# Performance work log

Measured on AMD Instinct MI355X. Metric: run time of the kernel, lower is better.

## Reference

```python
import jax, jax.numpy as jnp
import numpy as np

B, N, F = 4, 100000, 64   # batch, points per cloud, feature dim
S, K = 256, 8             # render size, points per pixel
RADIUS = 1.0
R = 2.0 * RADIUS / float(S)  # self.r in the torch module


def setup_inputs() -> dict:
    key = jax.random.key(0)
    k1, k2, k3, k4 = jax.random.split(key, 4)
    features = jax.random.normal(k1, (B, N, F), dtype=jnp.float32)
    # packed point indices (rasterizer output); all valid here
    idx = jax.random.randint(k2, (B, S, S, K), 0, B * N, dtype=jnp.int64)
    zbuf = jax.random.uniform(k3, (B, S, S, K), dtype=jnp.float32)
    # squared xy distances, scaled into [0, r^2) so exp weights are non-trivial
    dist_xy = jax.random.uniform(k4, (B, S, S, K), dtype=jnp.float32) * (R * R)
    return {"features": features, "idx": idx, "zbuf": zbuf, "dist_xy": dist_xy}


def reference(features, idx, zbuf, dist_xy):
    r = R
    # exponential_alpha: permute to (B, K, S, S), normalize by r^2, exp
    d = jnp.transpose(dist_xy, (0, 3, 1, 2))                 # B,K,S,S
    alpha = jnp.exp(-jnp.maximum(d / (r * r), 0.0))
    weights = jnp.clip(alpha, 0.0, 0.99)

    idx_p = jnp.transpose(idx, (0, 3, 1, 2))                 # B,K,S,S (long)
    valid = (idx_p >= 0).astype(features.dtype)

    feats_packed = features.reshape(B * N, F)                # packed features

    # alpha_composite: front-to-back over K with transmittance
    w_eff = weights * valid                                  # B,K,S,S
    trans = jnp.cumprod(1.0 - w_eff, axis=1)
    trans = jnp.concatenate([jnp.ones_like(trans[:, :1]), trans[:, :-1]], axis=1)
    contrib = w_eff * trans                                  # B,K,S,S

    safe_idx = jnp.clip(idx_p, 0, B * N - 1)
    out = jnp.zeros((B, F, S, S), dtype=features.dtype)
    for k in range(K):  # K is a small fixed constant (8)
        g = feats_packed[safe_idx[:, k]]                     # B,S,S,F gather
        out = out + jnp.transpose(g, (0, 3, 1, 2)) * contrib[:, k][:, None]

    # normalized depth: w_normed = (weights*valid) / sum_k, z_weighted
    w_sum = jnp.maximum(jnp.sum(w_eff, axis=1, keepdims=True), 1e-9)
    w_normed = w_eff / w_sum
    z = jnp.transpose(zbuf, (0, 3, 1, 2))                    # B,K,S,S
    depth = jnp.sum(z * w_normed, axis=1, keepdims=True)     # B,1,S,S

    # concat composited feats (B,F,S,S) with depth (B,1,S,S)
    return jnp.concatenate([out, depth], axis=1)
```

## Files before the change

kernel.cpp:

```cpp
#include <hip/hip_runtime.h>


#define BB 4
#define NN 100000
#define FF 64
#define SS 256
#define KK 8
#define BN (BB * NN)
#define RR_INV 16384.0f

__global__ __launch_bounds__(256)
void points_render_kernel(const float* __restrict__ features,
                          const int*   __restrict__ idx,
                          const float* __restrict__ zbuf,
                          const float* __restrict__ dist,
                          float* __restrict__ out)
{
    __shared__ float tile[64][FF + 1];
    __shared__ float s_contrib[64][KK];
    __shared__ int   s_off[64][KK];

    const int tid  = threadIdx.x;
    const int wave = tid >> 6;
    const int lane = tid & 63;

    const int blk = blockIdx.x;
    const int xb  = blk & 3;
    const int y   = (blk >> 2) & (SS - 1);
    const int b   = blk >> 10;
    const int x0  = xb * 64;

    const long long pixbase = (((long long)b * SS + y) * SS + x0);

    if (tid < 64) {
        const long long p = pixbase + tid;
        const float4* d4 = (const float4*)(dist + p * KK);
        const float4* z4 = (const float4*)(zbuf + p * KK);
        const int4*   i4 = (const int4*)(idx  + p * KK);
        float4 da = d4[0], db = d4[1];
        float4 za = z4[0], zb = z4[1];
        int4   ia = i4[0], ib = i4[1];

        float dd[KK] = {da.x, da.y, da.z, da.w, db.x, db.y, db.z, db.w};
        float zz[KK] = {za.x, za.y, za.z, za.w, zb.x, zb.y, zb.z, zb.w};
        int   ii[KK] = {ia.x, ia.y, ia.z, ia.w, ib.x, ib.y, ib.z, ib.w};

        float trans = 1.0f, wsum = 0.0f, depth = 0.0f;
        #pragma unroll
        for (int k = 0; k < KK; ++k) {
            float a  = __expf(-fmaxf(dd[k] * RR_INV, 0.0f));
            float we = fminf(a, 0.99f);
            if (ii[k] < 0) we = 0.0f;
            s_contrib[tid][k] = we * trans;
            trans *= (1.0f - we);
            wsum  += we;
            depth += zz[k] * we;

            int si = ii[k];
            si = si < 0 ? 0 : (si > BN - 1 ? BN - 1 : si);
            s_off[tid][k] = si * FF;
        }
        tile[tid][FF] = depth / fmaxf(wsum, 1e-9f);
    }
    __syncthreads();

    const float* fl = features + lane;

    #pragma unroll 4
    for (int i = 0; i < 16; ++i) {
        const int xl = wave * 16 + i;
        const float4 c0 = *(const float4*)&s_contrib[xl][0];
        const float4 c1 = *(const float4*)&s_contrib[xl][4];
        const int4   o0 = *(const int4*)&s_off[xl][0];
        const int4   o1 = *(const int4*)&s_off[xl][4];

        const float g0 = fl[o0.x], g1 = fl[o0.y], g2 = fl[o0.z], g3 = fl[o0.w];
        const float g4 = fl[o1.x], g5 = fl[o1.y], g6 = fl[o1.z], g7 = fl[o1.w];

        tile[xl][lane] = g0*c0.x + g1*c0.y + g2*c0.z + g3*c0.w
                       + g4*c1.x + g5*c1.y + g6*c1.z + g7*c1.w;
    }
    __syncthreads();

    float* outb = out + (long long)b * (FF + 1) * SS * SS + (long long)y * SS + x0;
    for (int j = tid; j < 64 * (FF + 1); j += 256) {
        const int c  = j >> 6;
        const int xl = j & 63;
        outb[(long long)c * (SS * SS) + xl] = tile[xl][c];
    }
}

extern "C" void kernel_launch(void* const* d_in, const int* in_sizes, int n_in,
                              void* d_out, int out_size, void* d_ws, size_t ws_size,
                              hipStream_t stream) {
    const float* features = (const float*)d_in[0];
    const int*   idx      = (const int*)d_in[1];
    const float* zbuf     = (const float*)d_in[2];
    const float* dist     = (const float*)d_in[3];
    float* out = (float*)d_out;

    const int nblocks = (BB * SS * SS) / 64;
    points_render_kernel<<<dim3(nblocks), dim3(256), 0, stream>>>(
        features, idx, zbuf, dist, out);
}
```

Measured before the change: 91.45 us.

## Gather features with float4 loads split across sub-wave groups and shuffle-reduce

Each wave now handles a pixel by splitting lanes into four groups of 16. Each group loads two of the K points' feature rows as 16-byte float4 vectors instead of eight scalar per-lane loads. Partial sums are combined with cross-lane xor shuffles. Contribution and byte offset are packed into one float2 in shared memory. This is meant to cut the number of load instructions and address computations, at the cost of eight shuffles per pixel and predicated LDS writes by only a quarter of the lanes. Byte offsets use 32-bit unsigned arithmetic, and BN*256 still fits in that range.

```diff
diff --git a/kernel.cpp b/kernel.cpp
--- a/kernel.cpp
+++ b/kernel.cpp
@@ -16,9 +16,8 @@
                           const float* __restrict__ dist,
                           float* __restrict__ out)
 {
-    __shared__ float tile[64][FF + 1];
-    __shared__ float s_contrib[64][KK];
-    __shared__ int   s_off[64][KK];
+    __shared__ float  tile[64][FF + 1];
+    __shared__ float2 s_oc[64][KK];
 
     const int tid  = threadIdx.x;
     const int wave = tid >> 6;
@@ -51,34 +50,57 @@
             float a  = __expf(-fmaxf(dd[k] * RR_INV, 0.0f));
             float we = fminf(a, 0.99f);
             if (ii[k] < 0) we = 0.0f;
-            s_contrib[tid][k] = we * trans;
+            float2 oc;
+            oc.x = we * trans;
             trans *= (1.0f - we);
             wsum  += we;
             depth += zz[k] * we;
 
             int si = ii[k];
             si = si < 0 ? 0 : (si > BN - 1 ? BN - 1 : si);
-            s_off[tid][k] = si * FF;
+            oc.y = __int_as_float(si << 8);
+            s_oc[tid][k] = oc;
         }
         tile[tid][FF] = depth / fmaxf(wsum, 1e-9f);
     }
     __syncthreads();
 
-    const float* fl = features + lane;
+    const int sub = lane >> 4;
+    const unsigned fb = (unsigned)((lane & 15) * 16);
+    const char* fbase = (const char*)features;
 
     #pragma unroll 4
     for (int i = 0; i < 16; ++i) {
         const int xl = wave * 16 + i;
-        const float4 c0 = *(const float4*)&s_contrib[xl][0];
-        const float4 c1 = *(const float4*)&s_contrib[xl][4];
-        const int4   o0 = *(const int4*)&s_off[xl][0];
-        const int4   o1 = *(const int4*)&s_off[xl][4];
+        const float2 e0 = s_oc[xl][sub];
+        const float2 e1 = s_oc[xl][sub + 4];
+        const unsigned o0 = (unsigned)__float_as_int(e0.y) + fb;
+        const unsigned o1 = (unsigned)__float_as_int(e1.y) + fb;
+        const float4 g0 = *(const float4*)(fbase + o0);
+        const float4 g1 = *(const float4*)(fbase + o1);
 
-        const float g0 = fl[o0.x], g1 = fl[o0.y], g2 = fl[o0.z], g3 = fl[o0.w];
-        const float g4 = fl[o1.x], g5 = fl[o1.y], g6 = fl[o1.z], g7 = fl[o1.w];
+        float4 acc;
+        acc.x = g0.x * e0.x + g1.x * e1.x;
+        acc.y = g0.y * e0.x + g1.y * e1.x;
+        acc.z = g0.z * e0.x + g1.z * e1.x;
+        acc.w = g0.w * e0.x + g1.w * e1.x;
 
-        tile[xl][lane] = g0*c0.x + g1*c0.y + g2*c0.z + g3*c0.w
-                       + g4*c1.x + g5*c1.y + g6*c1.z + g7*c1.w;
+        acc.x += __shfl_xor(acc.x, 16);
+        acc.y += __shfl_xor(acc.y, 16);
+        acc.z += __shfl_xor(acc.z, 16);
+        acc.w += __shfl_xor(acc.w, 16);
+        acc.x += __shfl_xor(acc.x, 32);
+        acc.y += __shfl_xor(acc.y, 32);
+        acc.z += __shfl_xor(acc.z, 32);
+        acc.w += __shfl_xor(acc.w, 32);
+
+        if (sub == 0) {
+            const int c = (lane & 15) * 4;
+            tile[xl][c + 0] = acc.x;
+            tile[xl][c + 1] = acc.y;
+            tile[xl][c + 2] = acc.z;
+            tile[xl][c + 3] = acc.w;
+        }
     }
     __syncthreads();
 
```

Measured after the change: 91.89 us. Within noise of the previous version (+0.5%).
